# Kernel tuning notes

Hardware: AMD Instinct MI355X
Metric: run time of the kernel (lower is better)

## Reference

```python
import jax, jax.numpy as jnp
import numpy as np

BS, QLEN, DIM, NH = 4, 2048, 1024, 16
DH = DIM // NH
NEG = float(np.finfo(np.float32).min)


def setup_inputs() -> dict:
    key = jax.random.key(0)
    ks = jax.random.split(key, 10)
    s = 1.0 / np.sqrt(DIM)
    return {
        "hidden_states": jax.random.normal(ks[0], (BS, QLEN, DIM), jnp.float32),
        "attention_mask": jnp.ones((BS, QLEN), jnp.int32),
        "Wq": jax.random.normal(ks[1], (DIM, DIM), jnp.float32) * s,
        "bq": jnp.zeros((DIM,), jnp.float32),
        "Wk": jax.random.normal(ks[2], (DIM, DIM), jnp.float32) * s,
        "bk": jnp.zeros((DIM,), jnp.float32),
        "Wv": jax.random.normal(ks[3], (DIM, DIM), jnp.float32) * s,
        "bv": jnp.zeros((DIM,), jnp.float32),
        "Wo": jax.random.normal(ks[4], (DIM, DIM), jnp.float32) * s,
        "bo": jnp.zeros((DIM,), jnp.float32),
    }


def _heads(x, bs):
    # [bs, len, dim] -> [bs, n_heads, len, dim_per_head]
    return x.reshape(bs, -1, NH, DH).transpose(0, 2, 1, 3)


def reference(hidden_states, attention_mask, Wq, bq, Wk, bk, Wv, bv, Wo, bo):
    bs, qlen, dim = hidden_states.shape
    q = _heads(hidden_states @ Wq.T + bq, bs) / jnp.sqrt(jnp.asarray(DH, hidden_states.dtype))
    k = _heads(hidden_states @ Wk.T + bk, bs)
    v = _heads(hidden_states @ Wv.T + bv, bs)
    scores = jnp.einsum("bhqd,bhkd->bhqk", q, k)  # [bs, nh, qlen, klen]
    mask = (attention_mask == 0)[:, None, None, :]  # [bs,1,1,klen]
    scores = jnp.where(mask, NEG, scores)
    weights = jax.nn.softmax(scores.astype(jnp.float32), axis=-1).astype(scores.dtype)
    context = jnp.einsum("bhqk,bhkd->bhqd", weights, v)
    context = context.transpose(0, 2, 1, 3).reshape(bs, qlen, dim)
    return context @ Wo.T + bo
```

## Files before the change

kernel.cpp:

```cpp
#include <hip/hip_runtime.h>
#include <hip/hip_bf16.h>

#define BS 4
#define QLEN 2048
#define DIM 1024
#define NH 16
#define DH 64

typedef __attribute__((ext_vector_type(8))) short bf16x8;
typedef __attribute__((ext_vector_type(4))) float f32x4;
typedef __attribute__((ext_vector_type(16))) float f32x16;
typedef __attribute__((ext_vector_type(2))) unsigned int u32x2;
typedef __attribute__((ext_vector_type(4))) unsigned int u32x4;
typedef unsigned short u16;
typedef unsigned int u32;
typedef unsigned long long u64;

#define LOG2E 1.44269504088896f

__device__ __forceinline__ u32 cvtpk_bf16(float lo, float hi) {
    u32 r;
    asm("v_cvt_pk_bf16_f32 %0, %1, %2" : "=v"(r) : "v"(lo), "v"(hi));
    return r;
}
__device__ __forceinline__ u16 f2bf_hw(float f) { return (u16)cvtpk_bf16(f, f); }

__device__ __forceinline__ void async_lds16(const void* gp, void* lp) {
    __builtin_amdgcn_global_load_lds(
        (const __attribute__((address_space(1))) u32*)(u64)gp,
        (__attribute__((address_space(3))) u32*)(u32)(u64)lp,
        16, 0, 0);
}

__global__ void cvt_fused(const float* __restrict__ H,
                          const float* __restrict__ W0, const float* __restrict__ W1,
                          const float* __restrict__ W2, const float* __restrict__ W3,
                          u16* __restrict__ Hb,
                          u16* __restrict__ D0, u16* __restrict__ D1,
                          u16* __restrict__ D2, u16* __restrict__ D3) {
    const int h4 = (BS * QLEN * DIM) / 4;
    int i = blockIdx.x * blockDim.x + threadIdx.x;
    const float* s;
    u16* d;
    int off;
    if (i < h4) { s = H; d = Hb; off = i; }
    else {
        int j = i - h4;
        int ws = j >> 18;
        off = j & 262143;
        s = ws == 0 ? W0 : ws == 1 ? W1 : ws == 2 ? W2 : W3;
        d = ws == 0 ? D0 : ws == 1 ? D1 : ws == 2 ? D2 : D3;
    }
    float4 v = ((const float4*)s)[off];
    uint2 o;
    o.x = cvtpk_bf16(v.x, v.y);
    o.y = cvtpk_bf16(v.z, v.w);
    ((uint2*)d)[off] = o;
}

__global__ void mask_prep(const int* __restrict__ mask, float* __restrict__ maskF,
                          int* __restrict__ flags) {
    const int tile = blockIdx.x;
    const int lane = threadIdx.x;
    const int idx = tile * 64 + lane;
    const int v = mask[idx];
    maskF[idx] = v ? 1.0f : 0.0f;
    u64 bal = __ballot(v == 0);
    if (lane == 0) flags[tile] = (bal != 0ull) ? 1 : 0;
}

__global__ __launch_bounds__(256) void gemm_qkv(
    const u16* __restrict__ Hb,
    const u16* __restrict__ Wq, const u16* __restrict__ Wk, const u16* __restrict__ Wv,
    const float* __restrict__ bq, const float* __restrict__ bk, const float* __restrict__ bvv,
    u16* __restrict__ Qb, u16* __restrict__ Kb, u16* __restrict__ Vt)
{
    __shared__ __align__(16) u16 As[128 * 32];
    __shared__ __align__(16) u16 Bs[128 * 32];
    const int z = blockIdx.z;
    const u16* W = z == 0 ? Wq : z == 1 ? Wk : Wv;
    const float* bias = z == 0 ? bq : z == 1 ? bk : bvv;
    const int t = threadIdx.x;
    const int w = t >> 6, lane = t & 63;
    const int lr = lane & 15, lg = lane >> 4;
    const int m0 = blockIdx.y * 128, n0 = blockIdx.x * 128;
    const int wm = (w >> 1) * 64, wn = (w & 1) * 64;
    const int srow = w * 16 + (lane >> 2);
    const int sk = (lane & 3) * 8;

    f32x4 acc[4][4] = {};

    for (int kt = 0; kt < DIM; kt += 32) {
        __syncthreads();
        async_lds16(Hb + (u64)(m0 + srow) * DIM + kt + sk,      &As[(w * 16) * 32]);
        async_lds16(Hb + (u64)(m0 + 64 + srow) * DIM + kt + sk, &As[(64 + w * 16) * 32]);
        async_lds16(W + (u64)(n0 + srow) * DIM + kt + sk,       &Bs[(w * 16) * 32]);
        async_lds16(W + (u64)(n0 + 64 + srow) * DIM + kt + sk,  &Bs[(64 + w * 16) * 32]);
        __syncthreads();
        bf16x8 a[4], b[4];
#pragma unroll
        for (int i = 0; i < 4; ++i) a[i] = *(const bf16x8*)&As[(wm + i * 16 + lr) * 32 + lg * 8];
#pragma unroll
        for (int i = 0; i < 4; ++i) b[i] = *(const bf16x8*)&Bs[(wn + i * 16 + lr) * 32 + lg * 8];
#pragma unroll
        for (int mi = 0; mi < 4; ++mi)
#pragma unroll
            for (int ni = 0; ni < 4; ++ni)
                acc[mi][ni] = __builtin_amdgcn_mfma_f32_16x16x32_bf16(a[mi], b[ni], acc[mi][ni], 0, 0, 0);
    }

#pragma unroll
    for (int mi = 0; mi < 4; ++mi)
#pragma unroll
        for (int ni = 0; ni < 4; ++ni) {
            const int col = n0 + wn + ni * 16 + lr;
            const float bb = bias[col];
#pragma unroll
            for (int r = 0; r < 4; ++r) {
                const int row = m0 + wm + mi * 16 + lg * 4 + r;
                const float v = acc[mi][ni][r] + bb;
                const int bh = (row >> 11) * NH + (col >> 6);
                const int q = row & (QLEN - 1);
                const int d = col & (DH - 1);
                if (z == 0)      Qb[((u64)bh * QLEN + q) * DH + d] = f2bf_hw(v * (0.125f * LOG2E));
                else if (z == 1) Kb[((u64)bh * QLEN + q) * DH + d] = f2bf_hw(v);
                else             Vt[((u64)bh * DH + d) * QLEN + q] = f2bf_hw(v);
            }
        }
}

__global__ __launch_bounds__(256) void gemm_o(
    const u16* __restrict__ A, const u16* __restrict__ W,
    const float* __restrict__ bias, float* __restrict__ ofp)
{
    __shared__ __align__(16) u16 As[128 * 32];
    __shared__ __align__(16) u16 Bs[128 * 32];
    const int t = threadIdx.x;
    const int w = t >> 6, lane = t & 63;
    const int lr = lane & 15, lg = lane >> 4;
    const int m0 = blockIdx.y * 128, n0 = blockIdx.x * 128;
    const int wm = (w >> 1) * 64, wn = (w & 1) * 64;
    const int srow = w * 16 + (lane >> 2);
    const int sk = (lane & 3) * 8;

    f32x4 acc[4][4] = {};

    for (int kt = 0; kt < DIM; kt += 32) {
        __syncthreads();
        async_lds16(A + (u64)(m0 + srow) * DIM + kt + sk,      &As[(w * 16) * 32]);
        async_lds16(A + (u64)(m0 + 64 + srow) * DIM + kt + sk, &As[(64 + w * 16) * 32]);
        async_lds16(W + (u64)(n0 + srow) * DIM + kt + sk,      &Bs[(w * 16) * 32]);
        async_lds16(W + (u64)(n0 + 64 + srow) * DIM + kt + sk, &Bs[(64 + w * 16) * 32]);
        __syncthreads();
        bf16x8 a[4], b[4];
#pragma unroll
        for (int i = 0; i < 4; ++i) a[i] = *(const bf16x8*)&As[(wm + i * 16 + lr) * 32 + lg * 8];
#pragma unroll
        for (int i = 0; i < 4; ++i) b[i] = *(const bf16x8*)&Bs[(wn + i * 16 + lr) * 32 + lg * 8];
#pragma unroll
        for (int mi = 0; mi < 4; ++mi)
#pragma unroll
            for (int ni = 0; ni < 4; ++ni)
                acc[mi][ni] = __builtin_amdgcn_mfma_f32_16x16x32_bf16(a[mi], b[ni], acc[mi][ni], 0, 0, 0);
    }

#pragma unroll
    for (int mi = 0; mi < 4; ++mi)
#pragma unroll
        for (int ni = 0; ni < 4; ++ni) {
            const int col = n0 + wn + ni * 16 + lr;
            const float bb = bias[col];
#pragma unroll
            for (int r = 0; r < 4; ++r) {
                const int row = m0 + wm + mi * 16 + lg * 4 + r;
                ofp[(u64)row * DIM + col] = acc[mi][ni][r] + bb;
            }
        }
}

__global__ __launch_bounds__(256) void attn_kernel(
    const u16* __restrict__ Qb, const u16* __restrict__ Kb, const u16* __restrict__ Vt,
    const float* __restrict__ maskF, const int* __restrict__ mflags, u16* __restrict__ ctx)
{
    __shared__ __align__(16) u16 Ks[2][64 * 64];
    __shared__ __align__(16) u16 Vs[2][64 * 64];

    const int t = threadIdx.x;
    const int w = t >> 6, lane = t & 63;
    const int l5 = lane & 31, hi = lane >> 5, l7 = lane & 7;

    const int id = blockIdx.x + 16 * blockIdx.y;
    const int v = (id & 7) * 128 + (id >> 3);
    const int qt = v & 15, bh = v >> 4;
    const int b = bh >> 4, hh = bh & 15;
    const int q0 = qt * 128;

    const u16* Kbh = Kb + (u64)bh * QLEN * DH;
    const u16* Vth = Vt + (u64)bh * DH * QLEN;
    const float* mFb = maskF + b * QLEN;
    const int* flb = mflags + b * (QLEN / 64);

    const u16* qp = Qb + ((u64)bh * QLEN + q0 + w * 32 + l5) * DH + hi * 8;
    bf16x8 bq[4];
#pragma unroll
    for (int dc = 0; dc < 4; ++dc) bq[dc] = *(const bf16x8*)(qp + dc * 16);

    f32x16 o[2] = {};
    float mrun = -3.0e38f, lsum = 0.f;

    const int srow = lane >> 3, schunk = lane & 7;

#define STAGE(BUF, KT) do {                                                            \
    _Pragma("unroll")                                                                  \
    for (int c = 0; c < 2; ++c) {                                                      \
        const int row_ = w * 16 + c * 8 + srow;                                        \
        const int ch_ = schunk ^ (row_ & 7);                                           \
        async_lds16(Kbh + (u64)((KT) + row_) * DH + ch_ * 8, &Ks[BUF][(w * 16 + c * 8) * 64]); \
        async_lds16(Vth + (u64)row_ * QLEN + (KT) + ch_ * 8, &Vs[BUF][(w * 16 + c * 8) * 64]); \
    } } while (0)

    STAGE(0, 0);
    __syncthreads();

    int buf = 0;
    for (int kt = 0; kt < QLEN; kt += 64) {
        if (kt + 64 < QLEN) STAGE(buf ^ 1, kt + 64);

        const char* Kbase = (const char*)&Ks[buf][0];
        const char* Vbase = (const char*)&Vs[buf][0];

        f32x16 s[2] = {};
#pragma unroll
        for (int dc = 0; dc < 4; ++dc) {
            const u32 off = (u32)(l5 * 128) + (u32)(((2 * dc + hi) ^ l7) << 4);
            bf16x8 ak0 = *(const bf16x8*)(Kbase + off);
            bf16x8 ak1 = *(const bf16x8*)(Kbase + off + 4096);
            s[0] = __builtin_amdgcn_mfma_f32_32x32x16_bf16(ak0, bq[dc], s[0], 0, 0, 0);
            s[1] = __builtin_amdgcn_mfma_f32_32x32x16_bf16(ak1, bq[dc], s[1], 0, 0, 0);
        }

        float mx[16];
#pragma unroll
        for (int i = 0; i < 16; ++i) mx[i] = fmaxf(s[0][i], s[1][i]);
#pragma unroll
        for (int st = 8; st > 0; st >>= 1)
#pragma unroll
            for (int i = 0; i < 16; ++i) if (i < st) mx[i] = fmaxf(mx[i], mx[i + st]);
        const float tma = fmaxf(mx[0], __shfl_xor(mx[0], 32));

        const float nm = fmaxf(mrun, tma);
        const float corr = exp2f(mrun - nm);
        mrun = nm;
        lsum *= corr;
#pragma unroll
        for (int i = 0; i < 16; ++i) { o[0][i] *= corr; o[1][i] *= corr; }

#pragma unroll
        for (int i = 0; i < 16; ++i) {
            s[0][i] = exp2f(s[0][i] - mrun);
            s[1][i] = exp2f(s[1][i] - mrun);
        }

        if (flb[kt >> 6]) {
#pragma unroll
            for (int kb = 0; kb < 2; ++kb)
#pragma unroll
                for (int m = 0; m < 4; ++m) {
                    float4 mm = *(const float4*)&mFb[kt + kb * 32 + m * 8 + hi * 4];
                    s[kb][4 * m + 0] *= mm.x;
                    s[kb][4 * m + 1] *= mm.y;
                    s[kb][4 * m + 2] *= mm.z;
                    s[kb][4 * m + 3] *= mm.w;
                }
        }

        {
            float ps[16];
#pragma unroll
            for (int i = 0; i < 16; ++i) ps[i] = s[0][i] + s[1][i];
#pragma unroll
            for (int st = 8; st > 0; st >>= 1)
#pragma unroll
                for (int i = 0; i < 16; ++i) if (i < st) ps[i] += ps[i + st];
            lsum += ps[0];
        }

#pragma unroll
        for (int kc = 0; kc < 4; ++kc) {
            const int kb = kc >> 1;
            const int base = 8 * (kc & 1);
            const u32 P00 = cvtpk_bf16(s[kb][base + 0], s[kb][base + 1]);
            const u32 P01 = cvtpk_bf16(s[kb][base + 2], s[kb][base + 3]);
            const u32 P10 = cvtpk_bf16(s[kb][base + 4], s[kb][base + 5]);
            const u32 P11 = cvtpk_bf16(s[kb][base + 6], s[kb][base + 7]);
            u32x2 w02 = __builtin_amdgcn_permlane32_swap(P00, P10, false, false);
            u32x2 w13 = __builtin_amdgcn_permlane32_swap(P01, P11, false, false);
            u32x4 words;
            words.x = w02[0]; words.y = w13[0]; words.z = w02[1]; words.w = w13[1];
            const bf16x8 bp = __builtin_bit_cast(bf16x8, words);

            const u32 voff = (u32)(l5 * 128) + (u32)(((2 * kc + hi) ^ l7) << 4);
            bf16x8 av0 = *(const bf16x8*)(Vbase + voff);
            bf16x8 av1 = *(const bf16x8*)(Vbase + voff + 4096);
            o[0] = __builtin_amdgcn_mfma_f32_32x32x16_bf16(av0, bp, o[0], 0, 0, 0);
            o[1] = __builtin_amdgcn_mfma_f32_32x32x16_bf16(av1, bp, o[1], 0, 0, 0);
        }

        __syncthreads();
        buf ^= 1;
    }
#undef STAGE

    const float lall = lsum + __shfl_xor(lsum, 32);
    const float inv = 1.0f / fmaxf(lall, 1e-37f);

    u16* cp = ctx + (((u64)b * QLEN + (q0 + w * 32 + l5)) * NH + hh) * DH;
#pragma unroll
    for (int db = 0; db < 2; ++db)
#pragma unroll
        for (int m = 0; m < 4; ++m) {
            const int d0 = db * 32 + m * 8 + hi * 4;
            const u32 wA = cvtpk_bf16(o[db][4 * m + 0] * inv, o[db][4 * m + 1] * inv);
            const u32 wB = cvtpk_bf16(o[db][4 * m + 2] * inv, o[db][4 * m + 3] * inv);
            *(u32*)(cp + d0) = wA;
            *(u32*)(cp + d0 + 2) = wB;
        }
}

extern "C" void kernel_launch(void* const* d_in, const int* in_sizes, int n_in,
                              void* d_out, int out_size, void* d_ws, size_t ws_size,
                              hipStream_t stream) {
    const float* H    = (const float*)d_in[0];
    const int*   mask = (const int*)d_in[1];
    const float* Wq   = (const float*)d_in[2];
    const float* bq   = (const float*)d_in[3];
    const float* Wk   = (const float*)d_in[4];
    const float* bk   = (const float*)d_in[5];
    const float* Wv   = (const float*)d_in[6];
    const float* bv   = (const float*)d_in[7];
    const float* Wo   = (const float*)d_in[8];
    const float* bo   = (const float*)d_in[9];
    float* out = (float*)d_out;

    const u64 NTOK = (u64)BS * QLEN;
    const u64 HN = NTOK * DIM;
    const u64 WN = (u64)DIM * DIM;

    u16* Hb  = (u16*)d_ws;
    u16* Wqb = Hb + HN;
    u16* Wkb = Wqb + WN;
    u16* Wvb = Wkb + WN;
    u16* Wob = Wvb + WN;
    u16* Qb  = Wob + WN;
    u16* Kb  = Qb + HN;
    u16* Vtg = Kb + HN;
    u16* Ctx = Vtg + HN;
    float* maskF = (float*)(Ctx + HN);
    int* mflags = (int*)(maskF + BS * QLEN);

    cvt_fused<<<12288, 256, 0, stream>>>(H, Wq, Wk, Wv, Wo, Hb, Wqb, Wkb, Wvb, Wob);
    mask_prep<<<BS * (QLEN / 64), 64, 0, stream>>>(mask, maskF, mflags);

    gemm_qkv<<<dim3(DIM / 128, (int)(NTOK / 128), 3), 256, 0, stream>>>(
        Hb, Wqb, Wkb, Wvb, bq, bk, bv, Qb, Kb, Vtg);

    attn_kernel<<<dim3(QLEN / 128, BS * NH), 256, 0, stream>>>(Qb, Kb, Vtg, maskF, mflags, Ctx);

    gemm_o<<<dim3(DIM / 128, (int)(NTOK / 128)), 256, 0, stream>>>(Ctx, Wob, bo, out);
}
```

Measured before the change: 269.5 us.

## Load K/V fragments directly from global memory and skip unneeded softmax rescaling

Drops the double-buffered LDS staging of K and V tiles along with the per-iteration block barrier. Each wave now loads its MFMA operand fragments straight from global memory into registers, relying on L2/L1 for reuse across the four waves. It also adds a lazy online-softmax rescale: the running max and output rescale are updated only when some lane's new tile max exceeds the old max by more than a threshold. The risks are redundant global traffic, since four waves read the same K/V, load latency no longer hidden by prefetch, and higher register pressure. The threshold keeps exponentials bounded, so accuracy should be preserved.

```diff
diff --git a/kernel.cpp b/kernel.cpp
--- a/kernel.cpp
+++ b/kernel.cpp
@@ -182,12 +182,9 @@
     const u16* __restrict__ Qb, const u16* __restrict__ Kb, const u16* __restrict__ Vt,
     const float* __restrict__ maskF, const int* __restrict__ mflags, u16* __restrict__ ctx)
 {
-    __shared__ __align__(16) u16 Ks[2][64 * 64];
-    __shared__ __align__(16) u16 Vs[2][64 * 64];
-
     const int t = threadIdx.x;
     const int w = t >> 6, lane = t & 63;
-    const int l5 = lane & 31, hi = lane >> 5, l7 = lane & 7;
+    const int l5 = lane & 31, hi = lane >> 5;
 
     const int id = blockIdx.x + 16 * blockIdx.y;
     const int v = (id & 7) * 128 + (id >> 3);
@@ -205,38 +202,33 @@
 #pragma unroll
     for (int dc = 0; dc < 4; ++dc) bq[dc] = *(const bf16x8*)(qp + dc * 16);
 
+    const u16* kbase0 = Kbh + (u64)l5 * DH + hi * 8;
+    const u16* vbase0 = Vth + (u64)l5 * QLEN + hi * 8;
+
     f32x16 o[2] = {};
     float mrun = -3.0e38f, lsum = 0.f;
 
-    const int srow = lane >> 3, schunk = lane & 7;
-
-#define STAGE(BUF, KT) do {                                                            \
-    _Pragma("unroll")                                                                  \
-    for (int c = 0; c < 2; ++c) {                                                      \
-        const int row_ = w * 16 + c * 8 + srow;                                        \
-        const int ch_ = schunk ^ (row_ & 7);                                           \
-        async_lds16(Kbh + (u64)((KT) + row_) * DH + ch_ * 8, &Ks[BUF][(w * 16 + c * 8) * 64]); \
-        async_lds16(Vth + (u64)row_ * QLEN + (KT) + ch_ * 8, &Vs[BUF][(w * 16 + c * 8) * 64]); \
-    } } while (0)
-
-    STAGE(0, 0);
-    __syncthreads();
-
-    int buf = 0;
     for (int kt = 0; kt < QLEN; kt += 64) {
-        if (kt + 64 < QLEN) STAGE(buf ^ 1, kt + 64);
-
-        const char* Kbase = (const char*)&Ks[buf][0];
-        const char* Vbase = (const char*)&Vs[buf][0];
+        const u16* kb0 = kbase0 + (u64)kt * DH;
+        bf16x8 ak[2][4];
+#pragma unroll
+        for (int dc = 0; dc < 4; ++dc) {
+            ak[0][dc] = *(const bf16x8*)(kb0 + dc * 16);
+            ak[1][dc] = *(const bf16x8*)(kb0 + 32 * DH + dc * 16);
+        }
+        const u16* vb0 = vbase0 + kt;
+        bf16x8 av[2][4];
+#pragma unroll
+        for (int db = 0; db < 2; ++db)
+#pragma unroll
+            for (int kc = 0; kc < 4; ++kc)
+                av[db][kc] = *(const bf16x8*)(vb0 + (u64)db * 32 * QLEN + kc * 16);
 
         f32x16 s[2] = {};
 #pragma unroll
         for (int dc = 0; dc < 4; ++dc) {
-            const u32 off = (u32)(l5 * 128) + (u32)(((2 * dc + hi) ^ l7) << 4);
-            bf16x8 ak0 = *(const bf16x8*)(Kbase + off);
-            bf16x8 ak1 = *(const bf16x8*)(Kbase + off + 4096);
-            s[0] = __builtin_amdgcn_mfma_f32_32x32x16_bf16(ak0, bq[dc], s[0], 0, 0, 0);
-            s[1] = __builtin_amdgcn_mfma_f32_32x32x16_bf16(ak1, bq[dc], s[1], 0, 0, 0);
+            s[0] = __builtin_amdgcn_mfma_f32_32x32x16_bf16(ak[0][dc], bq[dc], s[0], 0, 0, 0);
+            s[1] = __builtin_amdgcn_mfma_f32_32x32x16_bf16(ak[1][dc], bq[dc], s[1], 0, 0, 0);
         }
 
         float mx[16];
@@ -248,12 +240,14 @@
             for (int i = 0; i < 16; ++i) if (i < st) mx[i] = fmaxf(mx[i], mx[i + st]);
         const float tma = fmaxf(mx[0], __shfl_xor(mx[0], 32));
 
-        const float nm = fmaxf(mrun, tma);
-        const float corr = exp2f(mrun - nm);
-        mrun = nm;
-        lsum *= corr;
-#pragma unroll
-        for (int i = 0; i < 16; ++i) { o[0][i] *= corr; o[1][i] *= corr; }
+        if (!__all(tma <= mrun + 11.5415603f)) {
+            const float nm = fmaxf(mrun, tma);
+            const float corr = exp2f(mrun - nm);
+            mrun = nm;
+            lsum *= corr;
+#pragma unroll
+            for (int i = 0; i < 16; ++i) { o[0][i] *= corr; o[1][i] *= corr; }
+        }
 
 #pragma unroll
         for (int i = 0; i < 16; ++i) {
@@ -299,17 +293,10 @@
             words.x = w02[0]; words.y = w13[0]; words.z = w02[1]; words.w = w13[1];
             const bf16x8 bp = __builtin_bit_cast(bf16x8, words);
 
-            const u32 voff = (u32)(l5 * 128) + (u32)(((2 * kc + hi) ^ l7) << 4);
-            bf16x8 av0 = *(const bf16x8*)(Vbase + voff);
-            bf16x8 av1 = *(const bf16x8*)(Vbase + voff + 4096);
-            o[0] = __builtin_amdgcn_mfma_f32_32x32x16_bf16(av0, bp, o[0], 0, 0, 0);
-            o[1] = __builtin_amdgcn_mfma_f32_32x32x16_bf16(av1, bp, o[1], 0, 0, 0);
-        }
-
-        __syncthreads();
-        buf ^= 1;
+            o[0] = __builtin_amdgcn_mfma_f32_32x32x16_bf16(av[0][kc], bp, o[0], 0, 0, 0);
+            o[1] = __builtin_amdgcn_mfma_f32_32x32x16_bf16(av[1][kc], bp, o[1], 0, 0, 0);
+        }
     }
-#undef STAGE
 
     const float lall = lsum + __shfl_xor(lsum, 32);
     const float inv = 1.0f / fmaxf(lall, 1e-37f);
```

After: 367.6 us. 36.4% more time.
